# Kernel optimization log

Measured on AMD Instinct MI355X. Metric: run time of the kernel, lower is better.

Reference implementation:

```python
import jax, jax.numpy as jnp
import numpy as np

D_MODEL = 2048
NUM_HEADS = 16
D_K = D_MODEL // NUM_HEADS
MAX_SEQ_LEN = 2048


def setup_inputs() -> dict:
    key = jax.random.key(0)
    ks = jax.random.split(key, 9)
    s = 1.0 / np.sqrt(D_MODEL)
    x = jax.random.normal(ks[0], (4, 2048, D_MODEL), dtype=jnp.float32)
    Wq = jax.random.normal(ks[1], (D_MODEL, D_MODEL), dtype=jnp.float32) * s
    bq = jnp.zeros((D_MODEL,), dtype=jnp.float32)
    Wk = jax.random.normal(ks[2], (D_MODEL, D_MODEL), dtype=jnp.float32) * s
    bk = jnp.zeros((D_MODEL,), dtype=jnp.float32)
    Wv = jax.random.normal(ks[3], (D_MODEL, D_MODEL), dtype=jnp.float32) * s
    bv = jnp.zeros((D_MODEL,), dtype=jnp.float32)
    Wo = jax.random.normal(ks[4], (D_MODEL, D_MODEL), dtype=jnp.float32) * s
    bo = jnp.zeros((D_MODEL,), dtype=jnp.float32)
    return {"x": x, "Wq": Wq, "bq": bq, "Wk": Wk, "bk": bk,
            "Wv": Wv, "bv": bv, "Wo": Wo, "bo": bo}


def _rope_tables(seq_len, d_k, dtype):
    # GPT-NeoX style rotate-half RoPE tables: [seq_len, d_k]
    inv_freq = 1.0 / (10000.0 ** (np.arange(0, d_k, 2, dtype=np.float32) / d_k))
    pos = np.arange(seq_len, dtype=np.float32)
    freqs = np.outer(pos, inv_freq)              # [S, d_k/2]
    emb = np.concatenate([freqs, freqs], axis=-1)  # [S, d_k]
    return jnp.asarray(np.cos(emb), dtype=dtype), jnp.asarray(np.sin(emb), dtype=dtype)


def _apply_rope(x, cos, sin):
    # x: [B, H, S, d_k]; rotate-half
    x1, x2 = jnp.split(x, 2, axis=-1)
    rotated = jnp.concatenate([-x2, x1], axis=-1)
    return x * cos + rotated * sin


def reference(x, Wq, bq, Wk, bk, Wv, bv, Wo, bo):
    B, S, _ = x.shape
    cos, sin = _rope_tables(S, D_K, x.dtype)  # [S, d_k]

    def split_heads(t):  # [B,S,D] -> [B,H,S,d_k]
        return t.reshape(B, S, NUM_HEADS, D_K).transpose(0, 2, 1, 3)

    q = split_heads(x @ Wq.T + bq)
    k = split_heads(x @ Wk.T + bk)
    v = split_heads(x @ Wv.T + bv)

    q = _apply_rope(q, cos, sin)
    k = _apply_rope(k, cos, sin)

    scale = 1.0 / jnp.sqrt(jnp.asarray(D_K, dtype=x.dtype))
    scores = jnp.einsum("bhqd,bhkd->bhqk", q, k) * scale
    attn = jax.nn.softmax(scores, axis=-1)
    out = jnp.einsum("bhqk,bhkd->bhqd", attn, v)  # [B,H,S,d_k]
    out = out.transpose(0, 2, 1, 3).reshape(B, S, D_MODEL)
    return out @ Wo.T + bo
```

## Files before the change

kernel.cpp:

```cpp
#include <hip/hip_runtime.h>
#include <hip/hip_bf16.h>
#include <math.h>

typedef __bf16 bf16;
typedef __bf16 bf16x2 __attribute__((ext_vector_type(2)));
typedef __bf16 bf16x4 __attribute__((ext_vector_type(4)));
typedef __bf16 bf16x8 __attribute__((ext_vector_type(8)));
typedef float f32x4 __attribute__((ext_vector_type(4)));

#define D_MODEL 2048
#define SEQ 2048
#define BATCH 4
#define NH 16
#define DK 128

typedef const __attribute__((address_space(1))) void* as1_ptr;
typedef __attribute__((address_space(3))) void* as3_ptr;

__device__ __forceinline__ void gld_lds16(const bf16* g, bf16* l) {
  __builtin_amdgcn_global_load_lds((as1_ptr)g, (as3_ptr)l, 16, 0, 0);
}

extern "C" __device__ float __ocml_native_exp2_f32(float);
__device__ __forceinline__ float fast_exp2(float x) {
  return __ocml_native_exp2_f32(x);
}

__global__ void cvt_kernel(const float* __restrict__ in, bf16* __restrict__ out, int n8) {
  int i = blockIdx.x * 256 + threadIdx.x;
  if (i >= n8) return;
  long base = (long)i * 8;
  const float4* p = (const float4*)(in + base);
  float4 a = p[0], b = p[1];
  bf16x8 v;
  v[0] = (bf16)a.x; v[1] = (bf16)a.y; v[2] = (bf16)a.z; v[3] = (bf16)a.w;
  v[4] = (bf16)b.x; v[5] = (bf16)b.y; v[6] = (bf16)b.z; v[7] = (bf16)b.w;
  *(bf16x8*)(out + base) = v;
}

__global__ void cvt4_kernel(const float* a, const float* b, const float* c, const float* d,
                            bf16* oa, bf16* ob, bf16* oc, bf16* od) {
  const float* in; bf16* out;
  switch (blockIdx.y) {
    case 0: in = a; out = oa; break;
    case 1: in = b; out = ob; break;
    case 2: in = c; out = oc; break;
    default: in = d; out = od; break;
  }
  int i = blockIdx.x * 256 + threadIdx.x;
  long base = (long)i * 8;
  const float4* p = (const float4*)(in + base);
  float4 x = p[0], y = p[1];
  bf16x8 v;
  v[0] = (bf16)x.x; v[1] = (bf16)x.y; v[2] = (bf16)x.z; v[3] = (bf16)x.w;
  v[4] = (bf16)y.x; v[5] = (bf16)y.y; v[6] = (bf16)y.z; v[7] = (bf16)y.w;
  *(bf16x8*)(out + base) = v;
}

template<int OUT_F32, int BIAS_ROW>
__global__ __launch_bounds__(512, 2)
void gemm256(const bf16* __restrict__ A, const bf16* __restrict__ B,
             const float* __restrict__ bias, void* __restrict__ Cout, int K, int ldc)
{
  __shared__ alignas(16) bf16 As[2][256 * 64];
  __shared__ alignas(16) bf16 Bs[2][256 * 64];
  const int tid  = threadIdx.x;
  const int wave = tid >> 6, lane = tid & 63;
  const int quad = lane >> 4, l16 = lane & 15;
  const int n0 = blockIdx.x * 256, m0 = blockIdx.y * 256;
  const int wm = (wave >> 2) * 128, wn = (wave & 3) * 64;

  const bf16* Asrc[4]; const bf16* Bsrc[4];
  for (int i = 0; i < 4; i++) {
    int g = wave * 4 + i;
    int r = g * 8 + (lane >> 3);
    int c = (lane & 7) ^ (r & 7);
    Asrc[i] = A + (long)(m0 + r) * K + c * 8;
    Bsrc[i] = B + (long)(n0 + r) * K + c * 8;
  }

  f32x4 acc[8][4] = {};
  const int nt = K / 64;

  for (int i = 0; i < 4; i++) gld_lds16(Asrc[i],      &As[0][(wave * 4 + i) * 512]);
  for (int i = 0; i < 4; i++) gld_lds16(Bsrc[i],      &Bs[0][(wave * 4 + i) * 512]);
  for (int i = 0; i < 4; i++) gld_lds16(Asrc[i] + 64, &As[1][(wave * 4 + i) * 512]);
  for (int i = 0; i < 4; i++) gld_lds16(Bsrc[i] + 64, &Bs[1][(wave * 4 + i) * 512]);

  for (int t = 0; t < nt; t++) {
    const int cur = t & 1;
    asm volatile("s_waitcnt vmcnt(8)" ::: "memory");
    __builtin_amdgcn_s_barrier();
    const bf16* Ab = As[cur];
    const bf16* Bb = Bs[cur];

    bf16x8 Af[8], Bf[4];
    for (int mi = 0; mi < 8; mi++) {
      int ra = wm + mi * 16 + l16;
      int ch = quad ^ (ra & 7);
      Af[mi] = *(const bf16x8*)(&Ab[ra * 64 + ch * 8]);
    }
    for (int ni = 0; ni < 4; ni++) {
      int rb = wn + ni * 16 + l16;
      int ch = quad ^ (rb & 7);
      Bf[ni] = *(const bf16x8*)(&Bb[rb * 64 + ch * 8]);
    }
    asm volatile("s_waitcnt lgkmcnt(0)" ::: "memory");
    __builtin_amdgcn_sched_barrier(0);
    __builtin_amdgcn_s_setprio(1);
    for (int mi = 0; mi < 8; mi++)
      for (int ni = 0; ni < 4; ni++)
        acc[mi][ni] = __builtin_amdgcn_mfma_f32_16x16x32_bf16(Af[mi], Bf[ni], acc[mi][ni], 0, 0, 0);
    __builtin_amdgcn_s_setprio(0);

    for (int mi = 0; mi < 8; mi++) {
      int ra = wm + mi * 16 + l16;
      int ch = (4 + quad) ^ (ra & 7);
      Af[mi] = *(const bf16x8*)(&Ab[ra * 64 + ch * 8]);
    }
    for (int ni = 0; ni < 4; ni++) {
      int rb = wn + ni * 16 + l16;
      int ch = (4 + quad) ^ (rb & 7);
      Bf[ni] = *(const bf16x8*)(&Bb[rb * 64 + ch * 8]);
    }
    asm volatile("s_waitcnt lgkmcnt(0)" ::: "memory");
    __builtin_amdgcn_sched_barrier(0);
    __builtin_amdgcn_s_barrier();

    {
      long k0 = (long)((t + 2 < nt) ? (t + 2) : (nt - 1)) * 64;
      for (int i = 0; i < 4; i++) gld_lds16(Asrc[i] + k0, &As[cur][(wave * 4 + i) * 512]);
      for (int i = 0; i < 4; i++) gld_lds16(Bsrc[i] + k0, &Bs[cur][(wave * 4 + i) * 512]);
    }

    __builtin_amdgcn_s_setprio(1);
    for (int mi = 0; mi < 8; mi++)
      for (int ni = 0; ni < 4; ni++)
        acc[mi][ni] = __builtin_amdgcn_mfma_f32_16x16x32_bf16(Af[mi], Bf[ni], acc[mi][ni], 0, 0, 0);
    __builtin_amdgcn_s_setprio(0);
  }
  asm volatile("s_waitcnt vmcnt(0)" ::: "memory");

  float bv[4];
  if (!BIAS_ROW)
    for (int ni = 0; ni < 4; ni++) bv[ni] = bias[n0 + wn + ni * 16 + l16];
  for (int mi = 0; mi < 8; mi++)
    for (int r = 0; r < 4; r++) {
      long row = m0 + wm + mi * 16 + quad * 4 + r;
      float bm = BIAS_ROW ? bias[row] : 0.0f;
      for (int ni = 0; ni < 4; ni++) {
        float v = acc[mi][ni][r] + (BIAS_ROW ? bm : bv[ni]);
        long idx = row * (long)ldc + n0 + wn + ni * 16 + l16;
        if (OUT_F32) ((float*)Cout)[idx] = v;
        else         ((bf16*)Cout)[idx] = (bf16)v;
      }
    }
}

__global__ void ropetab_kernel(float* __restrict__ ctab) {
  int idx = blockIdx.x * 256 + threadIdx.x;
  int j = idx & 63, p = idx >> 6;
  float f = exp2f(-(float)j * 0.20762050593046f);
  float th = (float)p * f;
  ctab[idx * 2]     = cosf(th);
  ctab[idx * 2 + 1] = sinf(th);
}

__global__ void rope_kernel(bf16* __restrict__ Q, bf16* __restrict__ K,
                            const float* __restrict__ ctab) {
  long idx = (long)blockIdx.x * 256 + threadIdx.x;
  bf16* P = blockIdx.y ? K : Q;
  int i2 = (int)(idx & 31);
  int h  = (int)((idx >> 5) & 15);
  long row = idx >> 9;
  int pos = (int)(row & (SEQ - 1));
  float4 cs = *(const float4*)(ctab + ((long)pos * 64 + 2 * i2) * 2);
  long base = row * D_MODEL + h * DK + 2 * i2;
  bf16x2 x1 = *(bf16x2*)(P + base);
  bf16x2 x2 = *(bf16x2*)(P + base + 64);
  bf16x2 y1, y2;
  y1[0] = (bf16)((float)x1[0] * cs.x - (float)x2[0] * cs.y);
  y2[0] = (bf16)((float)x2[0] * cs.x + (float)x1[0] * cs.y);
  y1[1] = (bf16)((float)x1[1] * cs.z - (float)x2[1] * cs.w);
  y2[1] = (bf16)((float)x2[1] * cs.z + (float)x1[1] * cs.w);
  *(bf16x2*)(P + base)      = y1;
  *(bf16x2*)(P + base + 64) = y2;
}

__global__ __launch_bounds__(256, 2)
void attn_kernel(const bf16* __restrict__ Q, const bf16* __restrict__ K,
                 const bf16* __restrict__ Vt, bf16* __restrict__ O)
{
  __shared__ alignas(16) bf16 Ks[2][64 * 128];
  __shared__ alignas(16) bf16 Vts[2][128 * 64];
  __shared__ alignas(16) bf16 Ps[128 * 36];
  const int tid  = threadIdx.x;
  const int wave = tid >> 6, lane = tid & 63;
  const int quad = lane >> 4, l16 = lane & 15;
  const int qt = blockIdx.x, bh = blockIdx.y;
  const int b = bh >> 4, h = bh & 15;
  const long qrow0 = (long)b * SEQ + qt * 128;
  const bf16* Qb = Q + qrow0 * D_MODEL + h * DK;
  const bf16* Kb = K + (long)b * SEQ * D_MODEL + h * DK;
  const bf16* Vb = Vt + (long)(h * DK) * (BATCH * SEQ) + b * SEQ;

  bf16x8 Qf[2][4];
  for (int ni = 0; ni < 2; ni++)
    for (int ks = 0; ks < 4; ks++)
      Qf[ni][ks] = *(const bf16x8*)(Qb + (long)(wave * 32 + ni * 16 + l16) * D_MODEL + ks * 32 + quad * 8);

  const bf16* Ksrc[4]; const bf16* Vsrc[4];
  for (int i = 0; i < 4; i++) {
    int g = wave * 4 + i;
    int rk = 4 * g + (lane >> 4);
    int ck = l16 ^ (rk & 7);
    Ksrc[i] = Kb + (long)rk * D_MODEL + ck * 8;
    int rv = 8 * g + (lane >> 3);
    int cv = (lane & 7) ^ (rv & 7);
    Vsrc[i] = Vb + (long)rv * (BATCH * SEQ) + cv * 8;
  }

  f32x4 Oacc[8][2] = {};
  float lsum[2] = {0.0f, 0.0f};
  const float kSc = 0.088388347648318447f * 1.4426950408889634f;
  const int swz = l16 & 7;

  for (int i = 0; i < 4; i++) gld_lds16(Ksrc[i], &Ks[0][(wave * 4 + i) * 512]);
  for (int i = 0; i < 4; i++) gld_lds16(Vsrc[i], &Vts[0][(wave * 4 + i) * 512]);
  __syncthreads();

  int cur = 0;
  for (int kt = 64; kt <= SEQ; kt += 64) {
    if (kt < SEQ) {
      for (int i = 0; i < 4; i++)
        gld_lds16(Ksrc[i] + (long)kt * D_MODEL, &Ks[cur ^ 1][(wave * 4 + i) * 512]);
      for (int i = 0; i < 4; i++)
        gld_lds16(Vsrc[i] + kt, &Vts[cur ^ 1][(wave * 4 + i) * 512]);
    }
    const bf16* Ksb = Ks[cur];
    const bf16* Vsb = Vts[cur];

    for (int hh = 0; hh < 2; hh++) {
      f32x4 Sc[2][2] = {};
      __builtin_amdgcn_s_setprio(1);
      for (int ks = 0; ks < 4; ks++) {
        bf16x8 Kf[2];
        for (int j = 0; j < 2; j++) {
          int si = hh * 2 + j;
          int c = (ks * 4 + quad) ^ swz;
          Kf[j] = *(const bf16x8*)(&Ksb[(si * 16 + l16) * 128 + c * 8]);
        }
        for (int j = 0; j < 2; j++)
          for (int ni = 0; ni < 2; ni++)
            Sc[j][ni] = __builtin_amdgcn_mfma_f32_16x16x32_bf16(Kf[j], Qf[ni][ks], Sc[j][ni], 0, 0, 0);
      }
      __builtin_amdgcn_s_setprio(0);

      for (int j = 0; j < 2; j++)
        for (int ni = 0; ni < 2; ni++) {
          bf16x4 pk;
          for (int r = 0; r < 4; r++) {
            float p = fast_exp2(Sc[j][ni][r] * kSc);
            lsum[ni] += p;
            pk[r] = (bf16)p;
          }
          *(bf16x4*)(&Ps[(wave * 32 + ni * 16 + l16) * 36 + j * 16 + quad * 4]) = pk;
        }

      __builtin_amdgcn_s_setprio(1);
      bf16x8 Pf[2];
      for (int ni = 0; ni < 2; ni++)
        Pf[ni] = *(const bf16x8*)(&Ps[(wave * 32 + ni * 16 + l16) * 36 + quad * 8]);
      for (int mi = 0; mi < 8; mi++) {
        int c = (hh * 4 + quad) ^ swz;
        bf16x8 Vf = *(const bf16x8*)(&Vsb[(mi * 16 + l16) * 64 + c * 8]);
        for (int ni = 0; ni < 2; ni++)
          Oacc[mi][ni] = __builtin_amdgcn_mfma_f32_16x16x32_bf16(Vf, Pf[ni], Oacc[mi][ni], 0, 0, 0);
      }
      __builtin_amdgcn_s_setprio(0);
    }

    __syncthreads();
    cur ^= 1;
  }

  for (int ni = 0; ni < 2; ni++) {
    lsum[ni] += __shfl_xor(lsum[ni], 16);
    lsum[ni] += __shfl_xor(lsum[ni], 32);
  }

  for (int ni = 0; ni < 2; ni++) {
    float rinv = 1.0f / lsum[ni];
    long rowbase = (qrow0 + wave * 32 + ni * 16 + l16) * (long)D_MODEL + h * DK + quad * 4;
    for (int mi = 0; mi < 8; mi++) {
      bf16x4 o;
      for (int r = 0; r < 4; r++) o[r] = (bf16)(Oacc[mi][ni][r] * rinv);
      *(bf16x4*)(O + rowbase + mi * 16) = o;
    }
  }
}

extern "C" void kernel_launch(void* const* d_in, const int* in_sizes, int n_in,
                              void* d_out, int out_size, void* d_ws, size_t ws_size,
                              hipStream_t stream) {
  const float* x  = (const float*)d_in[0];
  const float* Wq = (const float*)d_in[1];
  const float* bq = (const float*)d_in[2];
  const float* Wk = (const float*)d_in[3];
  const float* bk = (const float*)d_in[4];
  const float* Wv = (const float*)d_in[5];
  const float* bv = (const float*)d_in[6];
  const float* Wo = (const float*)d_in[7];
  const float* bo = (const float*)d_in[8];
  float* out = (float*)d_out;

  bf16* ws = (bf16*)d_ws;
  bf16* xb  = ws;
  bf16* Wqb = ws + 16777216;
  bf16* Wkb = ws + 20971520;
  bf16* Wvb = ws + 25165824;
  bf16* Wob = ws + 29360128;
  bf16* Qp  = ws + 33554432;
  bf16* Kp  = ws + 50331648;
  bf16* VtF = ws + 67108864;
  float* ctab = (float*)ws;
  bf16* O   = xb;

  cvt_kernel<<<8192, 256, 0, stream>>>(x, xb, 2097152);
  cvt4_kernel<<<dim3(2048, 4), 256, 0, stream>>>(Wq, Wk, Wv, Wo, Wqb, Wkb, Wvb, Wob);

  gemm256<0, 0><<<dim3(8, 32), 512, 0, stream>>>(xb, Wqb, bq, Qp, 2048, 2048);
  gemm256<0, 0><<<dim3(8, 32), 512, 0, stream>>>(xb, Wkb, bk, Kp, 2048, 2048);
  gemm256<0, 1><<<dim3(32, 8), 512, 0, stream>>>(Wvb, xb, bv, VtF, 2048, 8192);

  ropetab_kernel<<<512, 256, 0, stream>>>(ctab);
  rope_kernel<<<dim3(16384, 2), 256, 0, stream>>>(Qp, Kp, ctab);

  attn_kernel<<<dim3(16, 64), 256, 0, stream>>>(Qp, Kp, VtF, O);

  gemm256<1, 0><<<dim3(8, 32), 512, 0, stream>>>(O, Wob, bo, out, 2048, 2048);
}
```

Baseline: 626.1 us.

## Restructure GEMM main loop into four-phase quadrant pipeline with split staging

Measured after the change: 626.3 us. Within noise of the previous version (+0.0%).

```diff
diff --git a/kernel.cpp b/kernel.cpp
--- a/kernel.cpp
+++ b/kernel.cpp
@@ -70,74 +70,85 @@
   const int n0 = blockIdx.x * 256, m0 = blockIdx.y * 256;
   const int wm = (wave >> 2) * 128, wn = (wave & 3) * 64;
 
-  const bf16* Asrc[4]; const bf16* Bsrc[4];
-  for (int i = 0; i < 4; i++) {
-    int g = wave * 4 + i;
-    int r = g * 8 + (lane >> 3);
-    int c = (lane & 7) ^ (r & 7);
-    Asrc[i] = A + (long)(m0 + r) * K + c * 8;
-    Bsrc[i] = B + (long)(n0 + r) * K + c * 8;
-  }
+  const bf16 *ApS[2][2], *BpS[2][2];
+  int gA[2][2], gB[2][2];
+  for (int s = 0; s < 2; s++)
+    for (int j = 0; j < 2; j++) {
+      int idx = wave * 2 + j;
+      int ga = (idx >> 3) * 16 + s * 8 + (idx & 7);
+      int ra = ga * 8 + (lane >> 3);
+      int ca = (lane & 7) ^ (ra & 7);
+      ApS[s][j] = A + (long)(m0 + ra) * K + ca * 8; gA[s][j] = ga;
+      int gb = (idx >> 2) * 8 + s * 4 + (idx & 3);
+      int rb = gb * 8 + (lane >> 3);
+      int cb = (lane & 7) ^ (rb & 7);
+      BpS[s][j] = B + (long)(n0 + rb) * K + cb * 8; gB[s][j] = gb;
+    }
+
+#define STAGE_A(T2, S) { long k0_ = (long)(T2) * 64; int b_ = (T2) & 1; \
+    for (int j = 0; j < 2; j++) gld_lds16(ApS[S][j] + k0_, &As[b_][gA[S][j] * 512]); }
+#define STAGE_B(T2, S) { long k0_ = (long)(T2) * 64; int b_ = (T2) & 1; \
+    for (int j = 0; j < 2; j++) gld_lds16(BpS[S][j] + k0_, &Bs[b_][gB[S][j] * 512]); }
+
+#define READ_A(AF, MH) \
+  for (int mi = 0; mi < 4; mi++) \
+    for (int ks = 0; ks < 2; ks++) { \
+      int ra_ = wm + ((MH) * 4 + mi) * 16 + l16; \
+      int ch_ = (ks * 4 + quad) ^ (ra_ & 7); \
+      AF[mi * 2 + ks] = *(const bf16x8*)(&Ab[ra_ * 64 + ch_ * 8]); \
+    }
+#define READ_B(BF, NHH) \
+  for (int ni = 0; ni < 2; ni++) \
+    for (int ks = 0; ks < 2; ks++) { \
+      int rb_ = wn + ((NHH) * 2 + ni) * 16 + l16; \
+      int ch_ = (ks * 4 + quad) ^ (rb_ & 7); \
+      BF[ni * 2 + ks] = *(const bf16x8*)(&Bb[rb_ * 64 + ch_ * 8]); \
+    }
+#define MFMA16(AF, BF, MH, NHH) \
+  for (int mi = 0; mi < 4; mi++) \
+    for (int ni = 0; ni < 2; ni++) \
+      for (int ks = 0; ks < 2; ks++) \
+        acc[(MH) * 4 + mi][(NHH) * 2 + ni] = __builtin_amdgcn_mfma_f32_16x16x32_bf16( \
+            AF[mi * 2 + ks], BF[ni * 2 + ks], acc[(MH) * 4 + mi][(NHH) * 2 + ni], 0, 0, 0);
+#define PHASE_MFMA(AF, BF, MH, NHH) \
+  __builtin_amdgcn_s_barrier(); \
+  asm volatile("s_waitcnt lgkmcnt(0)" ::: "memory"); \
+  __builtin_amdgcn_sched_barrier(0); \
+  __builtin_amdgcn_s_setprio(1); \
+  MFMA16(AF, BF, MH, NHH); \
+  __builtin_amdgcn_s_setprio(0); \
+  __builtin_amdgcn_s_barrier();
 
   f32x4 acc[8][4] = {};
   const int nt = K / 64;
 
-  for (int i = 0; i < 4; i++) gld_lds16(Asrc[i],      &As[0][(wave * 4 + i) * 512]);
-  for (int i = 0; i < 4; i++) gld_lds16(Bsrc[i],      &Bs[0][(wave * 4 + i) * 512]);
-  for (int i = 0; i < 4; i++) gld_lds16(Asrc[i] + 64, &As[1][(wave * 4 + i) * 512]);
-  for (int i = 0; i < 4; i++) gld_lds16(Bsrc[i] + 64, &Bs[1][(wave * 4 + i) * 512]);
+  STAGE_A(0, 0); STAGE_B(0, 1); STAGE_A(0, 1);
+  STAGE_B(0, 0); STAGE_A(1, 0); STAGE_B(1, 1); STAGE_A(1, 1);
 
   for (int t = 0; t < nt; t++) {
     const int cur = t & 1;
-    asm volatile("s_waitcnt vmcnt(8)" ::: "memory");
+    if (t < nt - 1) { asm volatile("s_waitcnt vmcnt(6)" ::: "memory"); }
+    else            { asm volatile("s_waitcnt vmcnt(0)" ::: "memory"); }
     __builtin_amdgcn_s_barrier();
     const bf16* Ab = As[cur];
     const bf16* Bb = Bs[cur];
-
-    bf16x8 Af[8], Bf[4];
-    for (int mi = 0; mi < 8; mi++) {
-      int ra = wm + mi * 16 + l16;
-      int ch = quad ^ (ra & 7);
-      Af[mi] = *(const bf16x8*)(&Ab[ra * 64 + ch * 8]);
-    }
-    for (int ni = 0; ni < 4; ni++) {
-      int rb = wn + ni * 16 + l16;
-      int ch = quad ^ (rb & 7);
-      Bf[ni] = *(const bf16x8*)(&Bb[rb * 64 + ch * 8]);
-    }
-    asm volatile("s_waitcnt lgkmcnt(0)" ::: "memory");
-    __builtin_amdgcn_sched_barrier(0);
-    __builtin_amdgcn_s_setprio(1);
-    for (int mi = 0; mi < 8; mi++)
-      for (int ni = 0; ni < 4; ni++)
-        acc[mi][ni] = __builtin_amdgcn_mfma_f32_16x16x32_bf16(Af[mi], Bf[ni], acc[mi][ni], 0, 0, 0);
-    __builtin_amdgcn_s_setprio(0);
-
-    for (int mi = 0; mi < 8; mi++) {
-      int ra = wm + mi * 16 + l16;
-      int ch = (4 + quad) ^ (ra & 7);
-      Af[mi] = *(const bf16x8*)(&Ab[ra * 64 + ch * 8]);
-    }
-    for (int ni = 0; ni < 4; ni++) {
-      int rb = wn + ni * 16 + l16;
-      int ch = (4 + quad) ^ (rb & 7);
-      Bf[ni] = *(const bf16x8*)(&Bb[rb * 64 + ch * 8]);
-    }
-    asm volatile("s_waitcnt lgkmcnt(0)" ::: "memory");
-    __builtin_amdgcn_sched_barrier(0);
-    __builtin_amdgcn_s_barrier();
-
-    {
-      long k0 = (long)((t + 2 < nt) ? (t + 2) : (nt - 1)) * 64;
-      for (int i = 0; i < 4; i++) gld_lds16(Asrc[i] + k0, &As[cur][(wave * 4 + i) * 512]);
-      for (int i = 0; i < 4; i++) gld_lds16(Bsrc[i] + k0, &Bs[cur][(wave * 4 + i) * 512]);
-    }
-
-    __builtin_amdgcn_s_setprio(1);
-    for (int mi = 0; mi < 8; mi++)
-      for (int ni = 0; ni < 4; ni++)
-        acc[mi][ni] = __builtin_amdgcn_mfma_f32_16x16x32_bf16(Af[mi], Bf[ni], acc[mi][ni], 0, 0, 0);
-    __builtin_amdgcn_s_setprio(0);
+    bf16x8 Af[8], Bf0[4], Bf1[4];
+
+    READ_A(Af, 0); READ_B(Bf0, 0);
+    if (t + 1 < nt) STAGE_B(t + 1, 0);
+    PHASE_MFMA(Af, Bf0, 0, 0);
+
+    READ_B(Bf1, 1);
+    if (t + 2 < nt) STAGE_A(t + 2, 0);
+    PHASE_MFMA(Af, Bf1, 0, 1);
+
+    READ_A(Af, 1);
+    if (t + 2 < nt) STAGE_B(t + 2, 1);
+    PHASE_MFMA(Af, Bf1, 1, 1);
+
+    READ_B(Bf0, 0);
+    if (t + 2 < nt) STAGE_A(t + 2, 1);
+    PHASE_MFMA(Af, Bf0, 1, 0);
   }
   asm volatile("s_waitcnt vmcnt(0)" ::: "memory");
 
@@ -155,6 +166,12 @@
         else         ((bf16*)Cout)[idx] = (bf16)v;
       }
     }
+#undef STAGE_A
+#undef STAGE_B
+#undef READ_A
+#undef READ_B
+#undef MFMA16
+#undef PHASE_MFMA
 }
 
 __global__ void ropetab_kernel(float* __restrict__ ctab) {
```
